# Kernel optimization log

Hardware: AMD Instinct MI355X
Metric: run time of the kernel (lower is better)

## Reference

```python
import jax, jax.numpy as jnp
import numpy as np

K = 3  # kernel size (filtr = [3, 3])


def _unfold(x, k):
    """torch.nn.functional.unfold equivalent for NCHW, stride=1, pad=0, dilation=1.
    Returns [N, C, k*k, L] with patch index ordered (kh, kw), matching torch."""
    N, C, H, Wd = x.shape
    oh, ow = H - k + 1, Wd - k + 1
    cols = [x[:, :, i:i + oh, j:j + ow] for i in range(k) for j in range(k)]
    xu = jnp.stack(cols, axis=2)              # [N, C, k*k, oh, ow]
    return xu.reshape(N, C, k * k, oh * ow)   # [N, C, KK, L]


def setup_inputs() -> dict:
    key = jax.random.key(0)
    k1, k2, k3 = jax.random.split(key, 3)
    N, C, H, Wd = 16, 16, 52, 52   # N must equal C for the module's B-broadcast to work
    O = 16                         # num_c
    x = jax.random.normal(k1, (N, C, H, Wd), dtype=jnp.float32)
    W = jax.random.normal(k2, (O, C, K * K, 1), dtype=jnp.float32)  # per-output, per-channel window weights
    B = jax.random.normal(k3, (O, C, 1), dtype=jnp.float32)         # bias
    return {"x": x, "W": W, "B": B}


def reference(x, W, B):
    # x: [N,C,H,W]; W: [O,C,KK,1]; B: [O,C,1]
    xu = _unfold(x, K)[:, None]                          # [N,1,C,KK,L]
    mul = xu * W[None]                                   # [N,O,C,KK,L]
    size = jnp.sum(W, axis=(-2, -1), keepdims=True)      # [O,C,1,1]  (xi = (-2,-1))
    mean = jnp.mean(mul, axis=(-2, -1), keepdims=True)   # [N,O,C,1,1]
    i = jnp.square(mul - mean) / size                    # weighted variance terms
    out = jnp.sum(i, axis=(-2, -1, -3))                  # x2 = (-2,-1,-3) -> [N,O]
    # sqrt=0 -> no sqrt. Bias add broadcasts (1,N,O) with (O,C,1) -> [O, N(=C), O]
    return out + B
```

## Files before the change

kernel.cpp:

```cpp
#include <hip/hip_runtime.h>

#define NN 16
#define CC 16
#define HH 52
#define WW 52
#define KKN 9
#define OO 16
#define INV_L2 (1.0f / 22500.0f)

__global__ __launch_bounds__(64) void tvar_stage1(const float* __restrict__ x,
                                                  float* __restrict__ T,
                                                  float* __restrict__ Q) {
    __shared__ float img[HH * WW];
    __shared__ float R[6][HH];
    __shared__ float colfull[6], e0[6], e1[6], e50[6], e51[6];

    const int nc = blockIdx.x;
    const int t  = threadIdx.x;

    const float4* src = (const float4*)(x + nc * (HH * WW));
    float4* dst = (float4*)img;
    for (int i = t; i < (HH * WW) / 4; i += 64) dst[i] = src[i];
    __syncthreads();

    if (t < HH) {
        const float* row = img + t * WW;
        float s = 0.f, s2 = 0.f;
        #pragma unroll
        for (int xc = 0; xc < WW; ++xc) { float v = row[xc]; s += v; s2 += v * v; }
        const float a0 = row[0], a1 = row[1], a50 = row[50], a51 = row[51];
        R[0][t] = s  - a50 - a51;
        R[1][t] = s  - a0  - a51;
        R[2][t] = s  - a0  - a1;
        R[3][t] = s2 - a50 * a50 - a51 * a51;
        R[4][t] = s2 - a0  * a0  - a51 * a51;
        R[5][t] = s2 - a0  * a0  - a1  * a1;
    }
    __syncthreads();

    if (t < 6) {
        float s = 0.f;
        for (int r = 0; r < HH; ++r) s += R[t][r];
        colfull[t] = s;
        e0[t] = R[t][0]; e1[t] = R[t][1]; e50[t] = R[t][50]; e51[t] = R[t][51];
    }
    __syncthreads();

    if (t < KKN) {
        const int i = t / 3, j = t % 3;
        const float c1 = (i == 0) ? (e50[j] + e51[j])
                       : (i == 1) ? (e0[j]  + e51[j])
                                  : (e0[j]  + e1[j]);
        T[nc * KKN + t] = colfull[j] - c1;
        const float c2 = (i == 0) ? (e50[3 + j] + e51[3 + j])
                       : (i == 1) ? (e0[3 + j]  + e51[3 + j])
                                  : (e0[3 + j]  + e1[3 + j]);
        Q[nc * KKN + t] = colfull[3 + j] - c2;
    }
}

__global__ __launch_bounds__(256) void tvar_stage2(const float* __restrict__ Wt,
                                                   const float* __restrict__ B,
                                                   const float* __restrict__ T,
                                                   const float* __restrict__ Q,
                                                   float* __restrict__ out) {
    __shared__ float sW[OO * CC * KKN];
    __shared__ float sT[NN * CC * KKN];
    __shared__ float sQ[NN * CC * KKN];

    const int t = threadIdx.x;
    for (int i = t; i < OO * CC * KKN; i += 256) {
        sW[i] = Wt[i];
        sT[i] = T[i];
        sQ[i] = Q[i];
    }
    __syncthreads();

    const int n = t >> 4;
    const int o = t & 15;

    float acc = 0.f;
    #pragma unroll
    for (int c = 0; c < CC; ++c) {
        const float* w = sW + (o * CC + c) * KKN;
        const float* tt = sT + (n * CC + c) * KKN;
        const float* qq = sQ + (n * CC + c) * KKN;
        float size = 0.f, s1 = 0.f, sq = 0.f;
        #pragma unroll
        for (int k = 0; k < KKN; ++k) {
            const float wv = w[k];
            size += wv;
            s1   += wv * tt[k];
            sq   += wv * wv * qq[k];
        }
        acc += (sq - s1 * s1 * INV_L2) / size;
    }

    #pragma unroll
    for (int i = 0; i < OO; ++i) {
        out[i * 256 + t] = acc + B[i * CC + n];
    }
}

extern "C" void kernel_launch(void* const* d_in, const int* in_sizes, int n_in,
                              void* d_out, int out_size, void* d_ws, size_t ws_size,
                              hipStream_t stream) {
    const float* x  = (const float*)d_in[0];
    const float* Wt = (const float*)d_in[1];
    const float* B  = (const float*)d_in[2];
    float* out = (float*)d_out;

    float* T = (float*)d_ws;
    float* Q = T + NN * CC * KKN;

    tvar_stage1<<<NN * CC, 64, 0, stream>>>(x, T, Q);
    tvar_stage2<<<1, 256, 0, stream>>>(Wt, B, T, Q, out);
}
```

Baseline: 67.98 us.

## Fuse two stages via last-block atomic counter into single kernel

Merges the per-image moment kernel and the final reduction kernel into one launch. The last block to finish, detected with an atomic counter after a threadfence, performs the final contraction using 64 threads handling 4 (n,o) pairs each. A memset resets the counter every call, and the image-load loop is unrolled. This removes one kernel launch and its inter-kernel gap, but adds a memset, a serialized tail on a single 64-thread block, and more shared memory per block, which may reduce occupancy of stage one.

```diff
diff --git a/kernel.cpp b/kernel.cpp
--- a/kernel.cpp
+++ b/kernel.cpp
@@ -6,28 +6,42 @@
 #define WW 52
 #define KKN 9
 #define OO 16
+#define NBLK (NN * CC)
 #define INV_L2 (1.0f / 22500.0f)
 
-__global__ __launch_bounds__(64) void tvar_stage1(const float* __restrict__ x,
-                                                  float* __restrict__ T,
-                                                  float* __restrict__ Q) {
+__global__ __launch_bounds__(64) void tvar_fused(const float* __restrict__ x,
+                                                 const float* __restrict__ Wt,
+                                                 const float* __restrict__ B,
+                                                 float* __restrict__ T,
+                                                 float* __restrict__ Q,
+                                                 int* __restrict__ counter,
+                                                 float* __restrict__ out) {
     __shared__ float img[HH * WW];
     __shared__ float R[6][HH];
     __shared__ float colfull[6], e0[6], e1[6], e50[6], e51[6];
+    __shared__ int   is_last;
+    __shared__ float sW[OO * CC * KKN];
+    __shared__ float sT[NN * CC * KKN];
+    __shared__ float sQ[NN * CC * KKN];
+    __shared__ float sB[OO * CC];
 
     const int nc = blockIdx.x;
     const int t  = threadIdx.x;
 
     const float4* src = (const float4*)(x + nc * (HH * WW));
     float4* dst = (float4*)img;
-    for (int i = t; i < (HH * WW) / 4; i += 64) dst[i] = src[i];
+    #pragma unroll
+    for (int i = 0; i < 11; ++i) {
+        const int idx = t + i * 64;
+        if (idx < (HH * WW) / 4) dst[idx] = src[idx];
+    }
     __syncthreads();
 
     if (t < HH) {
         const float* row = img + t * WW;
         float s = 0.f, s2 = 0.f;
         #pragma unroll
-        for (int xc = 0; xc < WW; ++xc) { float v = row[xc]; s += v; s2 += v * v; }
+        for (int xc = 0; xc < WW; ++xc) { const float v = row[xc]; s += v; s2 += v * v; }
         const float a0 = row[0], a1 = row[1], a50 = row[50], a51 = row[51];
         R[0][t] = s  - a50 - a51;
         R[1][t] = s  - a0  - a51;
@@ -57,48 +71,63 @@
                                   : (e0[3 + j]  + e1[3 + j]);
         Q[nc * KKN + t] = colfull[3 + j] - c2;
     }
-}
 
-__global__ __launch_bounds__(256) void tvar_stage2(const float* __restrict__ Wt,
-                                                   const float* __restrict__ B,
-                                                   const float* __restrict__ T,
-                                                   const float* __restrict__ Q,
-                                                   float* __restrict__ out) {
-    __shared__ float sW[OO * CC * KKN];
-    __shared__ float sT[NN * CC * KKN];
-    __shared__ float sQ[NN * CC * KKN];
+    __threadfence();
+    __syncthreads();
+    if (t == 0) {
+        const int old = __hip_atomic_fetch_add(counter, 1, __ATOMIC_ACQ_REL,
+                                               __HIP_MEMORY_SCOPE_AGENT);
+        is_last = (old == NBLK - 1) ? 1 : 0;
+    }
+    __syncthreads();
+    if (!is_last) return;
 
-    const int t = threadIdx.x;
-    for (int i = t; i < OO * CC * KKN; i += 256) {
-        sW[i] = Wt[i];
-        sT[i] = T[i];
-        sQ[i] = Q[i];
+    {
+        const float4* gw = (const float4*)Wt;
+        const float4* gt = (const float4*)T;
+        const float4* gq = (const float4*)Q;
+        for (int i = t; i < (OO * CC * KKN) / 4; i += 64) {
+            ((float4*)sW)[i] = gw[i];
+            ((float4*)sT)[i] = gt[i];
+            ((float4*)sQ)[i] = gq[i];
+        }
+        const float4* gb = (const float4*)B;
+        if (t < (OO * CC) / 4) ((float4*)sB)[t] = gb[t];
     }
     __syncthreads();
 
-    const int n = t >> 4;
-    const int o = t & 15;
-
-    float acc = 0.f;
+    float accv[4];
     #pragma unroll
-    for (int c = 0; c < CC; ++c) {
-        const float* w = sW + (o * CC + c) * KKN;
-        const float* tt = sT + (n * CC + c) * KKN;
-        const float* qq = sQ + (n * CC + c) * KKN;
-        float size = 0.f, s1 = 0.f, sq = 0.f;
+    for (int p = 0; p < 4; ++p) {
+        const int pair = t + p * 64;
+        const int n = pair >> 4;
+        const int o = pair & 15;
+        float acc = 0.f;
         #pragma unroll
-        for (int k = 0; k < KKN; ++k) {
-            const float wv = w[k];
-            size += wv;
-            s1   += wv * tt[k];
-            sq   += wv * wv * qq[k];
+        for (int c = 0; c < CC; ++c) {
+            const float* w  = sW + (o * CC + c) * KKN;
+            const float* tt = sT + (n * CC + c) * KKN;
+            const float* qq = sQ + (n * CC + c) * KKN;
+            float size = 0.f, s1 = 0.f, sq = 0.f;
+            #pragma unroll
+            for (int k = 0; k < KKN; ++k) {
+                const float wv = w[k];
+                size += wv;
+                s1   += wv * tt[k];
+                sq   += wv * wv * qq[k];
+            }
+            acc += (sq - s1 * s1 * INV_L2) / size;
         }
-        acc += (sq - s1 * s1 * INV_L2) / size;
+        accv[p] = acc;
     }
 
     #pragma unroll
     for (int i = 0; i < OO; ++i) {
-        out[i * 256 + t] = acc + B[i * CC + n];
+        #pragma unroll
+        for (int p = 0; p < 4; ++p) {
+            const int pair = t + p * 64;
+            out[i * 256 + pair] = accv[p] + sB[i * CC + (pair >> 4)];
+        }
     }
 }
 
@@ -110,9 +139,10 @@
     const float* B  = (const float*)d_in[2];
     float* out = (float*)d_out;
 
-    float* T = (float*)d_ws;
+    int*   counter = (int*)d_ws;
+    float* T = (float*)d_ws + 16;
     float* Q = T + NN * CC * KKN;
 
-    tvar_stage1<<<NN * CC, 64, 0, stream>>>(x, T, Q);
-    tvar_stage2<<<1, 256, 0, stream>>>(Wt, B, T, Q, out);
+    hipMemsetAsync(d_ws, 0, 64, stream);
+    tvar_fused<<<NBLK, 64, 0, stream>>>(x, Wt, B, T, Q, counter, out);
 }
```

New measurement: 82.72 us. 1.22x slower.

## Fuse both stages into one kernel with wavefront-shuffle column reductions

Applied to the files above, without the earlier changes.

Replaces the two-kernel pipeline with a single kernel that runs one block per batch item, using one wavefront per channel. Each lane sums one image column directly from global memory, and the per-image totals and edge terms come from wavefront shuffles instead of shared-memory staging. The per-output weighted variance is then computed in the same block, which removes the second launch and the workspace round trip. The cost is only 16 blocks of parallelism, strided column loads that are coalesced across lanes but not vectorised, and extra register pressure from the many shuffle results.

```diff
diff --git a/kernel.cpp b/kernel.cpp
--- a/kernel.cpp
+++ b/kernel.cpp
@@ -8,97 +8,113 @@
 #define OO 16
 #define INV_L2 (1.0f / 22500.0f)
 
-__global__ __launch_bounds__(64) void tvar_stage1(const float* __restrict__ x,
-                                                  float* __restrict__ T,
-                                                  float* __restrict__ Q) {
-    __shared__ float img[HH * WW];
-    __shared__ float R[6][HH];
-    __shared__ float colfull[6], e0[6], e1[6], e50[6], e51[6];
 
-    const int nc = blockIdx.x;
-    const int t  = threadIdx.x;
+#define REDUCE6(v, FULL, E0, E1, E50, E51)                                   \
+    {                                                                        \
+        E0 = __shfl((v), 0); E1 = __shfl((v), 1);                            \
+        E50 = __shfl((v), 50); E51 = __shfl((v), 51);                        \
+        float _s = (v);                                                      \
+        _s += __shfl_xor(_s, 32); _s += __shfl_xor(_s, 16);                  \
+        _s += __shfl_xor(_s, 8);  _s += __shfl_xor(_s, 4);                   \
+        _s += __shfl_xor(_s, 2);  _s += __shfl_xor(_s, 1);                   \
+        FULL = _s;                                                           \
+    }
 
-    const float4* src = (const float4*)(x + nc * (HH * WW));
-    float4* dst = (float4*)img;
-    for (int i = t; i < (HH * WW) / 4; i += 64) dst[i] = src[i];
-    __syncthreads();
+__global__ __launch_bounds__(1024) void tvar_onepass(const float* __restrict__ x,
+                                                     const float* __restrict__ Wt,
+                                                     const float* __restrict__ B,
+                                                     float* __restrict__ out) {
+    __shared__ float sW[OO * CC * KKN];
+    __shared__ float sB[OO * CC];
+    __shared__ float sT[CC][KKN];
+    __shared__ float sQ[CC][KKN];
+    __shared__ float partial[CC * OO];
+    __shared__ float accO[OO];
 
-    if (t < HH) {
-        const float* row = img + t * WW;
+    const int n = blockIdx.x;
+    const int t = threadIdx.x;
+    const int w = t >> 6;
+    const int l = t & 63;
+
+    if (t < (OO * CC * KKN) / 4) ((float4*)sW)[t] = ((const float4*)Wt)[t];
+    if (t < (OO * CC) / 4)       ((float4*)sB)[t] = ((const float4*)B)[t];
+
+    float v0 = 0.f, v1 = 0.f, v2 = 0.f, v3 = 0.f, v4 = 0.f, v5 = 0.f;
+    if (l < WW) {
+        const float* base = x + (n * CC + w) * (HH * WW) + l;
         float s = 0.f, s2 = 0.f;
+        float a0 = 0.f, a1 = 0.f, a50 = 0.f, a51 = 0.f;
         #pragma unroll
-        for (int xc = 0; xc < WW; ++xc) { float v = row[xc]; s += v; s2 += v * v; }
-        const float a0 = row[0], a1 = row[1], a50 = row[50], a51 = row[51];
-        R[0][t] = s  - a50 - a51;
-        R[1][t] = s  - a0  - a51;
-        R[2][t] = s  - a0  - a1;
-        R[3][t] = s2 - a50 * a50 - a51 * a51;
-        R[4][t] = s2 - a0  * a0  - a51 * a51;
-        R[5][t] = s2 - a0  * a0  - a1  * a1;
+        for (int r = 0; r < HH; ++r) {
+            const float v = base[r * WW];
+            s += v; s2 += v * v;
+            if (r == 0)  a0  = v;
+            if (r == 1)  a1  = v;
+            if (r == 50) a50 = v;
+            if (r == 51) a51 = v;
+        }
+        v0 = s  - a50 - a51;
+        v1 = s  - a0  - a51;
+        v2 = s  - a0  - a1;
+        v3 = s2 - a50 * a50 - a51 * a51;
+        v4 = s2 - a0  * a0  - a51 * a51;
+        v5 = s2 - a0  * a0  - a1  * a1;
+    }
+
+    float F0, F1, F2, F3, F4, F5;
+    float P0_0, P1_0, P50_0, P51_0, P0_1, P1_1, P50_1, P51_1;
+    float P0_2, P1_2, P50_2, P51_2, P0_3, P1_3, P50_3, P51_3;
+    float P0_4, P1_4, P50_4, P51_4, P0_5, P1_5, P50_5, P51_5;
+    REDUCE6(v0, F0, P0_0, P1_0, P50_0, P51_0);
+    REDUCE6(v1, F1, P0_1, P1_1, P50_1, P51_1);
+    REDUCE6(v2, F2, P0_2, P1_2, P50_2, P51_2);
+    REDUCE6(v3, F3, P0_3, P1_3, P50_3, P51_3);
+    REDUCE6(v4, F4, P0_4, P1_4, P50_4, P51_4);
+    REDUCE6(v5, F5, P0_5, P1_5, P50_5, P51_5);
+
+    if (l < KKN) {
+        const int i = l / 3, j = l % 3;
+        const float Fs   = (i == 0) ? F0    : (i == 1) ? F1    : F2;
+        const float A0s  = (i == 0) ? P0_0  : (i == 1) ? P0_1  : P0_2;
+        const float A1s  = (i == 0) ? P1_0  : (i == 1) ? P1_1  : P1_2;
+        const float C0s  = (i == 0) ? P50_0 : (i == 1) ? P50_1 : P50_2;
+        const float C1s  = (i == 0) ? P51_0 : (i == 1) ? P51_1 : P51_2;
+        const float Fq   = (i == 0) ? F3    : (i == 1) ? F4    : F5;
+        const float A0q  = (i == 0) ? P0_3  : (i == 1) ? P0_4  : P0_5;
+        const float A1q  = (i == 0) ? P1_3  : (i == 1) ? P1_4  : P1_5;
+        const float C0q  = (i == 0) ? P50_3 : (i == 1) ? P50_4 : P50_5;
+        const float C1q  = (i == 0) ? P51_3 : (i == 1) ? P51_4 : P51_5;
+        const float corrS = (j == 0) ? (C0s + C1s) : (j == 1) ? (A0s + C1s) : (A0s + A1s);
+        const float corrQ = (j == 0) ? (C0q + C1q) : (j == 1) ? (A0q + C1q) : (A0q + A1q);
+        sT[w][l] = Fs - corrS;
+        sQ[w][l] = Fq - corrQ;
     }
     __syncthreads();
 
-    if (t < 6) {
-        float s = 0.f;
-        for (int r = 0; r < HH; ++r) s += R[t][r];
-        colfull[t] = s;
-        e0[t] = R[t][0]; e1[t] = R[t][1]; e50[t] = R[t][50]; e51[t] = R[t][51];
-    }
-    __syncthreads();
-
-    if (t < KKN) {
-        const int i = t / 3, j = t % 3;
-        const float c1 = (i == 0) ? (e50[j] + e51[j])
-                       : (i == 1) ? (e0[j]  + e51[j])
-                                  : (e0[j]  + e1[j]);
-        T[nc * KKN + t] = colfull[j] - c1;
-        const float c2 = (i == 0) ? (e50[3 + j] + e51[3 + j])
-                       : (i == 1) ? (e0[3 + j]  + e51[3 + j])
-                                  : (e0[3 + j]  + e1[3 + j]);
-        Q[nc * KKN + t] = colfull[3 + j] - c2;
-    }
-}
-
-__global__ __launch_bounds__(256) void tvar_stage2(const float* __restrict__ Wt,
-                                                   const float* __restrict__ B,
-                                                   const float* __restrict__ T,
-                                                   const float* __restrict__ Q,
-                                                   float* __restrict__ out) {
-    __shared__ float sW[OO * CC * KKN];
-    __shared__ float sT[NN * CC * KKN];
-    __shared__ float sQ[NN * CC * KKN];
-
-    const int t = threadIdx.x;
-    for (int i = t; i < OO * CC * KKN; i += 256) {
-        sW[i] = Wt[i];
-        sT[i] = T[i];
-        sQ[i] = Q[i];
-    }
-    __syncthreads();
-
-    const int n = t >> 4;
-    const int o = t & 15;
-
-    float acc = 0.f;
-    #pragma unroll
-    for (int c = 0; c < CC; ++c) {
-        const float* w = sW + (o * CC + c) * KKN;
-        const float* tt = sT + (n * CC + c) * KKN;
-        const float* qq = sQ + (n * CC + c) * KKN;
+    if (t < CC * OO) {
+        const int c = t >> 4, o = t & 15;
+        const float* wp = sW + (o * CC + c) * KKN;
         float size = 0.f, s1 = 0.f, sq = 0.f;
         #pragma unroll
         for (int k = 0; k < KKN; ++k) {
-            const float wv = w[k];
+            const float wv = wp[k];
             size += wv;
-            s1   += wv * tt[k];
-            sq   += wv * wv * qq[k];
+            s1   += wv * sT[c][k];
+            sq   += wv * wv * sQ[c][k];
         }
-        acc += (sq - s1 * s1 * INV_L2) / size;
+        partial[t] = (sq - s1 * s1 * INV_L2) / size;
     }
-
-    #pragma unroll
-    for (int i = 0; i < OO; ++i) {
-        out[i * 256 + t] = acc + B[i * CC + n];
+    __syncthreads();
+    if (t < OO) {
+        float a = 0.f;
+        #pragma unroll
+        for (int c = 0; c < CC; ++c) a += partial[c * 16 + t];
+        accO[t] = a;
+    }
+    __syncthreads();
+    if (t < OO * OO) {
+        const int i = t >> 4, o = t & 15;
+        out[i * (NN * OO) + n * OO + o] = accO[o] + sB[i * CC + n];
     }
 }
 
@@ -110,9 +126,5 @@
     const float* B  = (const float*)d_in[2];
     float* out = (float*)d_out;
 
-    float* T = (float*)d_ws;
-    float* Q = T + NN * CC * KKN;
-
-    tvar_stage1<<<NN * CC, 64, 0, stream>>>(x, T, Q);
-    tvar_stage2<<<1, 256, 0, stream>>>(Wt, B, T, Q, out);
+    tvar_onepass<<<NN, 1024, 0, stream>>>(x, Wt, B, out);
 }
```

New measurement: 61.30 us. 9.8% less time.
